# Kernel optimization log

Hardware: AMD Instinct MI355X
Metric: run time of the kernel (lower is better)

## Reference

```python
import jax, jax.numpy as jnp
import numpy as np

NUM_HEADS = 16
D_MODEL = 1024
DK = D_MODEL // NUM_HEADS


def setup_inputs() -> dict:
    key = jax.random.key(0)
    kH, kq, kk, kv, ko = jax.random.split(key, 5)
    scale = 0.02
    return {
        "H": jax.random.normal(kH, (4, 2048, D_MODEL), dtype=jnp.float32),
        "Wq": jax.random.normal(kq, (D_MODEL, D_MODEL), dtype=jnp.float32) * scale,
        "Wk": jax.random.normal(kk, (D_MODEL, D_MODEL), dtype=jnp.float32) * scale,
        "Wv": jax.random.normal(kv, (D_MODEL, D_MODEL), dtype=jnp.float32) * scale,
        "Wo": jax.random.normal(ko, (D_MODEL, D_MODEL), dtype=jnp.float32) * scale,
    }


def reference(H, Wq, Wk, Wv, Wo):
    b, T, d = H.shape
    n, dk = NUM_HEADS, DK
    # projections -> [b, n, T, dk]
    def split_heads(x):
        return x.reshape(b, T, n, dk).transpose(0, 2, 1, 3)
    Q = split_heads(H @ Wq)
    K = split_heads(H @ Wk)
    V = split_heads(H @ Wv)
    scores = jnp.einsum("bntd,bnsd->bnts", Q, K) / jnp.sqrt(jnp.float32(dk))
    causal = jnp.tril(jnp.ones((T, T), dtype=bool))
    scores = jnp.where(causal[None, None], scores, -jnp.inf)
    attn = jax.nn.softmax(scores, axis=-1)  # dropout rate 0 -> identity
    out = jnp.einsum("bnts,bnsd->bntd", attn, V)  # [b, n, T, dk]
    out = out.transpose(0, 2, 1, 3).reshape(b, T, n * dk)
    return out @ Wo
```

## Files before the change

### kernel.cpp

```cpp
#include <hip/hip_runtime.h>
#include <hip/hip_bf16.h>

#define T_SEQ 2048
#define DM 1024
#define DM2 2048
#define NH 16
#define DKH 64
#define NBATCH 4
#define MROWS (NBATCH*T_SEQ)

typedef __attribute__((ext_vector_type(8))) short bf16x8;
typedef __attribute__((ext_vector_type(4))) short bf16x4;
typedef __attribute__((ext_vector_type(4))) float f32x4;
typedef __attribute__((ext_vector_type(4))) unsigned short u16x4;

#define NEG_INF (-__builtin_inff())

#if __has_builtin(__builtin_amdgcn_exp2f)
#define EXP2(x) __builtin_amdgcn_exp2f(x)
#else
#define EXP2(x) exp2f(x)
#endif

static __device__ __forceinline__ unsigned short f2bf(float f){
  union { float f; unsigned u; } v; v.f = f;
  unsigned r = v.u + 0x7fffu + ((v.u >> 16) & 1u);
  return (unsigned short)(r >> 16);
}

static __device__ __forceinline__ unsigned short f2bfc(float f){
  union { __hip_bfloat16 h; unsigned short u; } cv;
  cv.h = __float2bfloat16(f);
  return cv.u;
}

static __device__ __forceinline__ void gload_lds16(const void* g, void* l){
  __builtin_amdgcn_global_load_lds(
      (const __attribute__((address_space(1))) void*)g,
      (__attribute__((address_space(3))) void*)l, 16, 0, 0);
}

__global__ void convh(const float4* __restrict__ in, u16x4* __restrict__ out, int n4){
  for (int i = blockIdx.x*blockDim.x + threadIdx.x; i < n4; i += gridDim.x*blockDim.x){
    float4 v = in[i];
    u16x4 o;
    o[0] = f2bf(v.x); o[1] = f2bf(v.y); o[2] = f2bf(v.z); o[3] = f2bf(v.w);
    out[i] = o;
  }
}

__global__ void convw(const float* __restrict__ W0, const float* __restrict__ W1,
                      const float* __restrict__ W2, const float* __restrict__ W3,
                      unsigned short* __restrict__ O0, unsigned short* __restrict__ O1,
                      unsigned short* __restrict__ O2, unsigned short* __restrict__ O3)
{
  const float* W = (blockIdx.z==0)?W0:(blockIdx.z==1)?W1:(blockIdx.z==2)?W2:W3;
  unsigned short* O = (blockIdx.z==0)?O0:(blockIdx.z==1)?O1:(blockIdx.z==2)?O2:O3;
  const float sc = (blockIdx.z==0) ? 0.18033688f : 1.0f;
  __shared__ float t[32][33];
  const int nx = blockIdx.x*32, kx = blockIdx.y*32;
  const int tx = threadIdx.x, ty = threadIdx.y;
  #pragma unroll
  for (int i = 0; i < 4; ++i)
    t[ty + i*8][tx] = W[(size_t)(kx + ty + i*8)*DM + nx + tx];
  __syncthreads();
  #pragma unroll
  for (int i = 0; i < 4; ++i)
    O[(size_t)(nx + ty + i*8)*DM + kx + tx] = f2bf(t[tx][ty + i*8] * sc);
}

template<bool F32OUT>
__global__ __launch_bounds__(256) void gemm_bt(const unsigned short* __restrict__ A,
                                               const unsigned short* __restrict__ Bt,
                                               void* __restrict__ Cp,
                                               int M, int N, int K)
{
  __shared__ __attribute__((aligned(16))) unsigned short a_lds[128*64];
  __shared__ __attribute__((aligned(16))) unsigned short b_lds[128*64];
  const int tid = threadIdx.x;
  const int w = tid >> 6, l = tid & 63;
  const int g = l >> 4, lr = l & 15;
  const int wr = w >> 1, wc = w & 1;
  const int m0 = blockIdx.x * 128, n0 = blockIdx.y * 128;
  f32x4 acc[4][4] = {};
  const int nk = K >> 6;
  for (int ks = 0; ks < nk; ++ks){
    __syncthreads();
    const int k0 = ks << 6;
    #pragma unroll
    for (int i = 0; i < 4; ++i){
      int c = (w*4 + i)*64 + l;
      int row = c >> 3;
      int gc = (c & 7) ^ (row & 7);
      gload_lds16(A + (size_t)(m0 + row)*K + (k0 + gc*8), &a_lds[c*8]);
    }
    #pragma unroll
    for (int i = 0; i < 4; ++i){
      int c = (w*4 + i)*64 + l;
      int row = c >> 3;
      int gc = (c & 7) ^ (row & 7);
      gload_lds16(Bt + (size_t)(n0 + row)*K + (k0 + gc*8), &b_lds[c*8]);
    }
    __syncthreads();
    #pragma unroll
    for (int kc = 0; kc < 2; ++kc){
      bf16x8 af[4], bf_[4];
      #pragma unroll
      for (int mt = 0; mt < 4; ++mt){
        int row = wr*64 + mt*16 + lr;
        int off = row*128 + ((kc*64 + g*16) ^ ((row & 7) << 4));
        af[mt] = *(const bf16x8*)((const char*)a_lds + off);
      }
      #pragma unroll
      for (int nt = 0; nt < 4; ++nt){
        int row = wc*64 + nt*16 + lr;
        int off = row*128 + ((kc*64 + g*16) ^ ((row & 7) << 4));
        bf_[nt] = *(const bf16x8*)((const char*)b_lds + off);
      }
      #pragma unroll
      for (int mt = 0; mt < 4; ++mt)
        #pragma unroll
        for (int nt = 0; nt < 4; ++nt)
          acc[mt][nt] = __builtin_amdgcn_mfma_f32_16x16x32_bf16(af[mt], bf_[nt], acc[mt][nt], 0, 0, 0);
    }
  }
  #pragma unroll
  for (int mt = 0; mt < 4; ++mt){
    #pragma unroll
    for (int nt = 0; nt < 4; ++nt){
      const int col = n0 + wc*64 + nt*16 + lr;
      #pragma unroll
      for (int r = 0; r < 4; ++r){
        const int row = m0 + wr*64 + mt*16 + 4*g + r;
        if (F32OUT) ((float*)Cp)[(size_t)row*N + col] = acc[mt][nt][r];
        else ((unsigned short*)Cp)[(size_t)row*N + col] = f2bf(acc[mt][nt][r]);
      }
    }
  }
}

static __device__ __forceinline__ void softmax_tile8(
    f32x4 (&s)[8], float& m_run, float& l_run, f32x4 (&acc)[4],
    bf16x4 (&pb)[8], int j0, int qg, int g, bool fullTile)
{
  if (!fullTile){
    #pragma unroll
    for (int kc = 0; kc < 8; ++kc)
      #pragma unroll
      for (int r = 0; r < 4; ++r){
        int kvg = j0 + kc*16 + 4*g + r;
        s[kc][r] = (kvg <= qg) ? s[kc][r] : NEG_INF;
      }
  }
  float m4[8];
  #pragma unroll
  for (int kc = 0; kc < 8; ++kc)
    m4[kc] = fmaxf(fmaxf(s[kc][0], s[kc][1]), fmaxf(s[kc][2], s[kc][3]));
  float tm = fmaxf(fmaxf(fmaxf(m4[0], m4[1]), fmaxf(m4[2], m4[3])),
                   fmaxf(fmaxf(m4[4], m4[5]), fmaxf(m4[6], m4[7])));
  tm = fmaxf(tm, __shfl_xor(tm, 16));
  tm = fmaxf(tm, __shfl_xor(tm, 32));
  float mm;
  if (__all(tm - m_run <= 8.f)){
    mm = m_run;
  } else {
    const float m_new = fmaxf(m_run, tm);
    const float fac = EXP2(m_run - m_new);
    l_run *= fac;
    m_run = m_new; mm = m_new;
    #pragma unroll
    for (int mt = 0; mt < 4; ++mt){
      acc[mt][0] *= fac; acc[mt][1] *= fac; acc[mt][2] *= fac; acc[mt][3] *= fac;
    }
  }
  float ps0 = 0.f, ps1 = 0.f, ps2 = 0.f, ps3 = 0.f;
  #pragma unroll
  for (int kc = 0; kc < 8; ++kc){
    float e0 = EXP2(s[kc][0] - mm); float e1 = EXP2(s[kc][1] - mm);
    float e2 = EXP2(s[kc][2] - mm); float e3 = EXP2(s[kc][3] - mm);
    s[kc][0] = e0; s[kc][1] = e1; s[kc][2] = e2; s[kc][3] = e3;
    ps0 += e0; ps1 += e1; ps2 += e2; ps3 += e3;
  }
  float ps = (ps0 + ps1) + (ps2 + ps3);
  ps += __shfl_xor(ps, 16);
  ps += __shfl_xor(ps, 32);
  l_run += ps;
  #pragma unroll
  for (int kc = 0; kc < 8; ++kc){
    bf16x4 t;
    t[0] = (short)f2bfc(s[kc][0]); t[1] = (short)f2bfc(s[kc][1]);
    t[2] = (short)f2bfc(s[kc][2]); t[3] = (short)f2bfc(s[kc][3]);
    pb[kc] = t;
  }
}

__global__ __launch_bounds__(512, 4) void attn_kernel(const unsigned short* __restrict__ QK,
                                                      const unsigned short* __restrict__ Vt,
                                                      unsigned short* __restrict__ Og)
{
  __shared__ __attribute__((aligned(16))) unsigned short k_lds[2][128*64];
  __shared__ __attribute__((aligned(16))) unsigned short v_lds[2][64*128];
  const int tid = threadIdx.x;
  const int w = tid >> 6, l = tid & 63;
  const int g = l >> 4, lr = l & 15;
  const int L = blockIdx.x;
  const int xcd = L & 7, idx = L >> 3;
  const int bh = xcd*8 + (idx & 7);
  const int pair = idx >> 3;
  const int b = bh >> 4, h = bh & 15;
  const size_t baseK = (size_t)(b*T_SEQ)*DM2 + 1024 + h*DKH;
  const size_t baseV = (size_t)(h*DKH)*MROWS + (size_t)b*T_SEQ;

  const int cA = tid, cB = tid + 512;
  const int krA = cA >> 3, kgA = (cA & 7) ^ (krA & 7);
  const int krB = cB >> 3, kgB = (cB & 7) ^ (krB & 7);
  const int vrA = cA >> 4, vgA = (cA & 15) ^ (vrA & 15);
  const int vrB = cB >> 4, vgB = (cB & 15) ^ (vrB & 15);

  auto STAGE = [&](int jt, int buf){
    const int j0s = jt * 128;
    gload_lds16(QK + baseK + (size_t)(j0s + krA)*DM2 + kgA*8, &k_lds[buf][cA*8]);
    gload_lds16(QK + baseK + (size_t)(j0s + krB)*DM2 + kgB*8, &k_lds[buf][cB*8]);
    gload_lds16(Vt + baseV + (size_t)vrA*MROWS + j0s + vgA*8, &v_lds[buf][cA*8]);
    gload_lds16(Vt + baseV + (size_t)vrB*MROWS + j0s + vgB*8, &v_lds[buf][cB*8]);
  };

  #pragma unroll 1
  for (int seg = 0; seg < 2; ++seg){
    const int qblk = seg ? pair : (15 - pair);
    const int q0 = qblk * 128;
    const int qlo = q0 + w*16;
    const int qg = qlo + lr;
    const size_t rowQ = (size_t)(b*T_SEQ + qg)*DM2 + h*DKH;
    bf16x8 qf[2];
    qf[0] = *(const bf16x8*)(QK + rowQ + g*8);
    qf[1] = *(const bf16x8*)(QK + rowQ + 32 + g*8);
    float m_run = NEG_INF, l_run = 0.f;
    f32x4 acc[4] = {};
    const int ntiles = qblk + 1;

    STAGE(0, 0);
    __syncthreads();

    for (int jt = 0; jt < ntiles; ++jt){
      const int cur = jt & 1;
      if (jt + 1 < ntiles) STAGE(jt + 1, cur ^ 1);
      const int j0 = jt * 128;

      f32x4 s[8];
      __builtin_amdgcn_s_setprio(1);
      #pragma unroll
      for (int kc = 0; kc < 8; ++kc){
        f32x4 z = {};
        #pragma unroll
        for (int c2 = 0; c2 < 2; ++c2){
          int row = kc*16 + lr;
          int off = row*128 + ((c2*64 + g*16) ^ ((row & 7) << 4));
          bf16x8 kf = *(const bf16x8*)((const char*)k_lds[cur] + off);
          z = __builtin_amdgcn_mfma_f32_16x16x32_bf16(kf, qf[c2], z, 0, 0, 0);
        }
        s[kc] = z;
      }
      __builtin_amdgcn_s_setprio(0);
      bf16x4 pb[8];
      softmax_tile8(s, m_run, l_run, acc, pb, j0, qg, g, jt < qblk);
      __builtin_amdgcn_s_setprio(1);
      #pragma unroll
      for (int mt = 0; mt < 4; ++mt){
        const int vrow = mt*16 + lr;
        #pragma unroll
        for (int kc = 0; kc < 8; ++kc){
          const int voff = vrow*256 + ((((kc<<1) + (g>>1)) ^ (vrow & 15)) << 4) + ((g & 1) << 3);
          bf16x4 vf = *(const bf16x4*)((const char*)v_lds[cur] + voff);
          acc[mt] = __builtin_amdgcn_mfma_f32_16x16x16bf16_1k(vf, pb[kc], acc[mt], 0, 0, 0);
        }
      }
      __builtin_amdgcn_s_setprio(0);
      __syncthreads();
    }
    const float inv = 1.f / l_run;
    const size_t rowO = (size_t)(b*T_SEQ + qg)*DM + h*DKH;
    #pragma unroll
    for (int mt = 0; mt < 4; ++mt){
      unsigned u0 = (unsigned)f2bfc(acc[mt][0]*inv) | ((unsigned)f2bfc(acc[mt][1]*inv) << 16);
      unsigned u1 = (unsigned)f2bfc(acc[mt][2]*inv) | ((unsigned)f2bfc(acc[mt][3]*inv) << 16);
      *(unsigned*)(Og + rowO + mt*16 + 4*g)     = u0;
      *(unsigned*)(Og + rowO + mt*16 + 4*g + 2) = u1;
    }
  }
}

extern "C" void kernel_launch(void* const* d_in, const int* in_sizes, int n_in,
                              void* d_out, int out_size, void* d_ws, size_t ws_size,
                              hipStream_t stream)
{
  (void)in_sizes; (void)n_in; (void)out_size; (void)ws_size;
  const float* H  = (const float*)d_in[0];
  const float* Wq = (const float*)d_in[1];
  const float* Wk = (const float*)d_in[2];
  const float* Wv = (const float*)d_in[3];
  const float* Wo = (const float*)d_in[4];
  char* ws = (char*)d_ws;
  unsigned short* Hb   = (unsigned short*)(ws);
  unsigned short* Wqkt = (unsigned short*)(ws + 16777216);
  unsigned short* Wkt  = (unsigned short*)(ws + 18874368);
  unsigned short* Wvt  = (unsigned short*)(ws + 20971520);
  unsigned short* Wot  = (unsigned short*)(ws + 23068672);
  unsigned short* QKb  = (unsigned short*)(ws + 25165824);
  unsigned short* Vtb  = (unsigned short*)(ws + 58720256);
  unsigned short* Ab   = (unsigned short*)(ws + 75497472);

  convh<<<2048, 256, 0, stream>>>((const float4*)H, (u16x4*)Hb, MROWS*DM/4);
  convw<<<dim3(32,32,4), dim3(32,8), 0, stream>>>(Wq, Wk, Wv, Wo, Wqkt, Wkt, Wvt, Wot);
  gemm_bt<false><<<dim3(64,16), 256, 0, stream>>>(Hb, Wqkt, QKb, MROWS, DM2, DM);
  gemm_bt<false><<<dim3(8,64), 256, 0, stream>>>(Wvt, Hb, Vtb, DM, MROWS, DM);
  attn_kernel<<<dim3(512), 512, 0, stream>>>(QKb, Vtb, Ab);
  gemm_bt<true><<<dim3(64,8), 256, 0, stream>>>(Ab, Wot, d_out, MROWS, DM, DM);
}
```

Before: 181.7 us.

## Merge prep and QKV GEMM launches, compute softmax denominator via MFMA, unroll attention loop

Merges the H and weight conversion kernels into one launch, and merges the QK and V-transpose GEMMs into a single grid, removing two launches and their tail gaps. In attention, the running row sum is no longer built with VALU adds and cross-lane shuffles. A fifth accumulator instead receives an extra MFMA against a ones vector, so the denominator comes out of the matrix unit. The KV loop is also unrolled by two with compile-time buffer indices. The ones-MFMA sums bf16-rounded probabilities rather than fp32 ones, which slightly changes numerics.

```diff
diff --git a/kernel.cpp b/kernel.cpp
--- a/kernel.cpp
+++ b/kernel.cpp
@@ -40,48 +40,51 @@
       (__attribute__((address_space(3))) void*)l, 16, 0, 0);
 }
 
-__global__ void convh(const float4* __restrict__ in, u16x4* __restrict__ out, int n4){
-  for (int i = blockIdx.x*blockDim.x + threadIdx.x; i < n4; i += gridDim.x*blockDim.x){
-    float4 v = in[i];
-    u16x4 o;
-    o[0] = f2bf(v.x); o[1] = f2bf(v.y); o[2] = f2bf(v.z); o[3] = f2bf(v.w);
-    out[i] = o;
-  }
-}
-
-__global__ void convw(const float* __restrict__ W0, const float* __restrict__ W1,
-                      const float* __restrict__ W2, const float* __restrict__ W3,
-                      unsigned short* __restrict__ O0, unsigned short* __restrict__ O1,
-                      unsigned short* __restrict__ O2, unsigned short* __restrict__ O3)
-{
-  const float* W = (blockIdx.z==0)?W0:(blockIdx.z==1)?W1:(blockIdx.z==2)?W2:W3;
-  unsigned short* O = (blockIdx.z==0)?O0:(blockIdx.z==1)?O1:(blockIdx.z==2)?O2:O3;
-  const float sc = (blockIdx.z==0) ? 0.18033688f : 1.0f;
+__global__ __launch_bounds__(256) void convprep(
+    const float* __restrict__ H,
+    const float* __restrict__ W0, const float* __restrict__ W1,
+    const float* __restrict__ W2, const float* __restrict__ W3,
+    u16x4* __restrict__ Hb4,
+    unsigned short* __restrict__ O0, unsigned short* __restrict__ O1,
+    unsigned short* __restrict__ O2, unsigned short* __restrict__ O3)
+{
   __shared__ float t[32][33];
-  const int nx = blockIdx.x*32, kx = blockIdx.y*32;
-  const int tx = threadIdx.x, ty = threadIdx.y;
-  #pragma unroll
-  for (int i = 0; i < 4; ++i)
-    t[ty + i*8][tx] = W[(size_t)(kx + ty + i*8)*DM + nx + tx];
-  __syncthreads();
-  #pragma unroll
-  for (int i = 0; i < 4; ++i)
-    O[(size_t)(nx + ty + i*8)*DM + kx + tx] = f2bf(t[tx][ty + i*8] * sc);
+  const int bid = blockIdx.x, tid = threadIdx.x;
+  if (bid < 4096){
+    const int z = bid >> 10, rem = bid & 1023;
+    const int nx = (rem & 31)*32, kx = (rem >> 5)*32;
+    const float* W = (z==0)?W0:(z==1)?W1:(z==2)?W2:W3;
+    unsigned short* O = (z==0)?O0:(z==1)?O1:(z==2)?O2:O3;
+    const float sc = (z==0) ? 0.18033688f : 1.0f;
+    const int tx = tid & 31, ty = tid >> 5;
+    #pragma unroll
+    for (int i = 0; i < 4; ++i)
+      t[ty + i*8][tx] = W[(size_t)(kx + ty + i*8)*DM + nx + tx];
+    __syncthreads();
+    #pragma unroll
+    for (int i = 0; i < 4; ++i)
+      O[(size_t)(nx + ty + i*8)*DM + kx + tx] = f2bf(t[tx][ty + i*8] * sc);
+  } else {
+    const int n4 = MROWS*DM/4;
+    for (int i = (bid - 4096)*256 + tid; i < n4; i += 2048*256){
+      float4 v = ((const float4*)H)[i];
+      u16x4 o;
+      o[0] = f2bf(v.x); o[1] = f2bf(v.y); o[2] = f2bf(v.z); o[3] = f2bf(v.w);
+      Hb4[i] = o;
+    }
+  }
 }
 
 template<bool F32OUT>
-__global__ __launch_bounds__(256) void gemm_bt(const unsigned short* __restrict__ A,
-                                               const unsigned short* __restrict__ Bt,
-                                               void* __restrict__ Cp,
-                                               int M, int N, int K)
-{
-  __shared__ __attribute__((aligned(16))) unsigned short a_lds[128*64];
-  __shared__ __attribute__((aligned(16))) unsigned short b_lds[128*64];
+static __device__ __forceinline__ void gemm_body(
+    const unsigned short* __restrict__ A, const unsigned short* __restrict__ Bt,
+    void* __restrict__ Cp, int N, int K, int m0, int n0,
+    unsigned short* a_lds, unsigned short* b_lds)
+{
   const int tid = threadIdx.x;
   const int w = tid >> 6, l = tid & 63;
   const int g = l >> 4, lr = l & 15;
   const int wr = w >> 1, wc = w & 1;
-  const int m0 = blockIdx.x * 128, n0 = blockIdx.y * 128;
   f32x4 acc[4][4] = {};
   const int nk = K >> 6;
   for (int ks = 0; ks < nk; ++ks){
@@ -139,8 +142,37 @@
   }
 }
 
+__global__ __launch_bounds__(256) void gemm_qkv(
+    const unsigned short* __restrict__ Hb, const unsigned short* __restrict__ Wqkt,
+    unsigned short* __restrict__ QKb,
+    const unsigned short* __restrict__ Wvt, unsigned short* __restrict__ Vtb)
+{
+  __shared__ __attribute__((aligned(16))) unsigned short a_lds[128*64];
+  __shared__ __attribute__((aligned(16))) unsigned short b_lds[128*64];
+  const int bid = blockIdx.x;
+  const unsigned short *A, *Bt; unsigned short* Cp; int N, m0, n0;
+  if (bid < 1024){
+    A = Hb; Bt = Wqkt; Cp = QKb; N = DM2;
+    m0 = (bid & 63)*128; n0 = (bid >> 6)*128;
+  } else {
+    const int t2 = bid - 1024;
+    A = Wvt; Bt = Hb; Cp = Vtb; N = MROWS;
+    m0 = (t2 & 7)*128; n0 = (t2 >> 3)*128;
+  }
+  gemm_body<false>(A, Bt, Cp, N, DM, m0, n0, a_lds, b_lds);
+}
+
+__global__ __launch_bounds__(256) void gemm_out(
+    const unsigned short* __restrict__ Ab, const unsigned short* __restrict__ Wot,
+    float* __restrict__ Out)
+{
+  __shared__ __attribute__((aligned(16))) unsigned short a_lds[128*64];
+  __shared__ __attribute__((aligned(16))) unsigned short b_lds[128*64];
+  gemm_body<true>(Ab, Wot, Out, DM, DM, blockIdx.x*128, blockIdx.y*128, a_lds, b_lds);
+}
+
 static __device__ __forceinline__ void softmax_tile8(
-    f32x4 (&s)[8], float& m_run, float& l_run, f32x4 (&acc)[4],
+    f32x4 (&s)[8], float& m_run, f32x4 (&acc)[5],
     bf16x4 (&pb)[8], int j0, int qg, int g, bool fullTile)
 {
   if (!fullTile){
@@ -166,30 +198,19 @@
   } else {
     const float m_new = fmaxf(m_run, tm);
     const float fac = EXP2(m_run - m_new);
-    l_run *= fac;
     m_run = m_new; mm = m_new;
     #pragma unroll
-    for (int mt = 0; mt < 4; ++mt){
+    for (int mt = 0; mt < 5; ++mt){
       acc[mt][0] *= fac; acc[mt][1] *= fac; acc[mt][2] *= fac; acc[mt][3] *= fac;
     }
   }
-  float ps0 = 0.f, ps1 = 0.f, ps2 = 0.f, ps3 = 0.f;
   #pragma unroll
   for (int kc = 0; kc < 8; ++kc){
     float e0 = EXP2(s[kc][0] - mm); float e1 = EXP2(s[kc][1] - mm);
     float e2 = EXP2(s[kc][2] - mm); float e3 = EXP2(s[kc][3] - mm);
-    s[kc][0] = e0; s[kc][1] = e1; s[kc][2] = e2; s[kc][3] = e3;
-    ps0 += e0; ps1 += e1; ps2 += e2; ps3 += e3;
-  }
-  float ps = (ps0 + ps1) + (ps2 + ps3);
-  ps += __shfl_xor(ps, 16);
-  ps += __shfl_xor(ps, 32);
-  l_run += ps;
-  #pragma unroll
-  for (int kc = 0; kc < 8; ++kc){
     bf16x4 t;
-    t[0] = (short)f2bfc(s[kc][0]); t[1] = (short)f2bfc(s[kc][1]);
-    t[2] = (short)f2bfc(s[kc][2]); t[3] = (short)f2bfc(s[kc][3]);
+    t[0] = (short)f2bfc(e0); t[1] = (short)f2bfc(e1);
+    t[2] = (short)f2bfc(e2); t[3] = (short)f2bfc(e3);
     pb[kc] = t;
   }
 }
@@ -210,6 +231,7 @@
   const int b = bh >> 4, h = bh & 15;
   const size_t baseK = (size_t)(b*T_SEQ)*DM2 + 1024 + h*DKH;
   const size_t baseV = (size_t)(h*DKH)*MROWS + (size_t)b*T_SEQ;
+  const bf16x4 vone = {(short)0x3F80, (short)0x3F80, (short)0x3F80, (short)0x3F80};
 
   const int cA = tid, cB = tid + 512;
   const int krA = cA >> 3, kgA = (cA & 7) ^ (krA & 7);
@@ -225,60 +247,71 @@
     gload_lds16(Vt + baseV + (size_t)vrB*MROWS + j0s + vgB*8, &v_lds[buf][cB*8]);
   };
 
+#define ROUND(JT, CUR) do{                                                       \
+    const int jt_ = (JT);                                                        \
+    if (jt_ + 1 < ntiles) STAGE(jt_ + 1, (CUR)^1);                               \
+    const int j0_ = jt_ * 128;                                                   \
+    f32x4 s[8];                                                                  \
+    __builtin_amdgcn_s_setprio(1);                                               \
+    _Pragma("unroll")                                                            \
+    for (int kc = 0; kc < 8; ++kc){                                              \
+      f32x4 z = {};                                                              \
+      _Pragma("unroll")                                                          \
+      for (int c2 = 0; c2 < 2; ++c2){                                            \
+        int row = kc*16 + lr;                                                    \
+        int off = row*128 + ((c2*64 + g*16) ^ ((row & 7) << 4));                 \
+        bf16x8 kf = *(const bf16x8*)((const char*)k_lds[CUR] + off);             \
+        z = __builtin_amdgcn_mfma_f32_16x16x32_bf16(kf, qf[c2], z, 0, 0, 0);     \
+      }                                                                          \
+      s[kc] = z;                                                                 \
+    }                                                                            \
+    __builtin_amdgcn_s_setprio(0);                                               \
+    bf16x4 pb[8];                                                                \
+    softmax_tile8(s, m_run, acc, pb, j0_, qg, g, jt_ < qblk);                    \
+    __builtin_amdgcn_s_setprio(1);                                               \
+    _Pragma("unroll")                                                            \
+    for (int mt = 0; mt < 4; ++mt){                                              \
+      const int vrow = mt*16 + lr;                                               \
+      _Pragma("unroll")                                                          \
+      for (int kc = 0; kc < 8; ++kc){                                            \
+        const int voff = vrow*256 + ((((kc<<1) + (g>>1)) ^ (vrow & 15)) << 4)    \
+                         + ((g & 1) << 3);                                       \
+        bf16x4 vf = *(const bf16x4*)((const char*)v_lds[CUR] + voff);            \
+        acc[mt] = __builtin_amdgcn_mfma_f32_16x16x16bf16_1k(vf, pb[kc], acc[mt], 0, 0, 0); \
+      }                                                                          \
+    }                                                                            \
+    _Pragma("unroll")                                                            \
+    for (int kc = 0; kc < 8; ++kc)                                               \
+      acc[4] = __builtin_amdgcn_mfma_f32_16x16x16bf16_1k(vone, pb[kc], acc[4], 0, 0, 0); \
+    __builtin_amdgcn_s_setprio(0);                                               \
+    __syncthreads();                                                             \
+  } while(0)
+
   #pragma unroll 1
   for (int seg = 0; seg < 2; ++seg){
     const int qblk = seg ? pair : (15 - pair);
     const int q0 = qblk * 128;
-    const int qlo = q0 + w*16;
-    const int qg = qlo + lr;
+    const int qg = q0 + w*16 + lr;
     const size_t rowQ = (size_t)(b*T_SEQ + qg)*DM2 + h*DKH;
     bf16x8 qf[2];
     qf[0] = *(const bf16x8*)(QK + rowQ + g*8);
     qf[1] = *(const bf16x8*)(QK + rowQ + 32 + g*8);
-    float m_run = NEG_INF, l_run = 0.f;
-    f32x4 acc[4] = {};
+    float m_run = NEG_INF;
+    f32x4 acc[5] = {};
     const int ntiles = qblk + 1;
 
     STAGE(0, 0);
     __syncthreads();
 
-    for (int jt = 0; jt < ntiles; ++jt){
-      const int cur = jt & 1;
-      if (jt + 1 < ntiles) STAGE(jt + 1, cur ^ 1);
-      const int j0 = jt * 128;
-
-      f32x4 s[8];
-      __builtin_amdgcn_s_setprio(1);
-      #pragma unroll
-      for (int kc = 0; kc < 8; ++kc){
-        f32x4 z = {};
-        #pragma unroll
-        for (int c2 = 0; c2 < 2; ++c2){
-          int row = kc*16 + lr;
-          int off = row*128 + ((c2*64 + g*16) ^ ((row & 7) << 4));
-          bf16x8 kf = *(const bf16x8*)((const char*)k_lds[cur] + off);
-          z = __builtin_amdgcn_mfma_f32_16x16x32_bf16(kf, qf[c2], z, 0, 0, 0);
-        }
-        s[kc] = z;
-      }
-      __builtin_amdgcn_s_setprio(0);
-      bf16x4 pb[8];
-      softmax_tile8(s, m_run, l_run, acc, pb, j0, qg, g, jt < qblk);
-      __builtin_amdgcn_s_setprio(1);
-      #pragma unroll
-      for (int mt = 0; mt < 4; ++mt){
-        const int vrow = mt*16 + lr;
-        #pragma unroll
-        for (int kc = 0; kc < 8; ++kc){
-          const int voff = vrow*256 + ((((kc<<1) + (g>>1)) ^ (vrow & 15)) << 4) + ((g & 1) << 3);
-          bf16x4 vf = *(const bf16x4*)((const char*)v_lds[cur] + voff);
-          acc[mt] = __builtin_amdgcn_mfma_f32_16x16x16bf16_1k(vf, pb[kc], acc[mt], 0, 0, 0);
-        }
-      }
-      __builtin_amdgcn_s_setprio(0);
-      __syncthreads();
-    }
-    const float inv = 1.f / l_run;
+    int jt = 0;
+    #pragma unroll 1
+    for (; jt + 2 <= ntiles; jt += 2){
+      ROUND(jt, 0);
+      ROUND(jt + 1, 1);
+    }
+    if (jt < ntiles) ROUND(jt, 0);
+
+    const float inv = 1.f / acc[4][0];
     const size_t rowO = (size_t)(b*T_SEQ + qg)*DM + h*DKH;
     #pragma unroll
     for (int mt = 0; mt < 4; ++mt){
@@ -288,6 +321,7 @@
       *(unsigned*)(Og + rowO + mt*16 + 4*g + 2) = u1;
     }
   }
+#undef ROUND
 }
 
 extern "C" void kernel_launch(void* const* d_in, const int* in_sizes, int n_in,
@@ -310,10 +344,9 @@
   unsigned short* Vtb  = (unsigned short*)(ws + 58720256);
   unsigned short* Ab   = (unsigned short*)(ws + 75497472);
 
-  convh<<<2048, 256, 0, stream>>>((const float4*)H, (u16x4*)Hb, MROWS*DM/4);
-  convw<<<dim3(32,32,4), dim3(32,8), 0, stream>>>(Wq, Wk, Wv, Wo, Wqkt, Wkt, Wvt, Wot);
-  gemm_bt<false><<<dim3(64,16), 256, 0, stream>>>(Hb, Wqkt, QKb, MROWS, DM2, DM);
-  gemm_bt<false><<<dim3(8,64), 256, 0, stream>>>(Wvt, Hb, Vtb, DM, MROWS, DM);
+  convprep<<<6144, 256, 0, stream>>>(H, Wq, Wk, Wv, Wo,
+                                     (u16x4*)Hb, Wqkt, Wkt, Wvt, Wot);
+  gemm_qkv<<<1536, 256, 0, stream>>>(Hb, Wqkt, QKb, Wvt, Vtb);
   attn_kernel<<<dim3(512), 512, 0, stream>>>(QKb, Vtb, Ab);
-  gemm_bt<true><<<dim3(64,8), 256, 0, stream>>>(Ab, Wot, d_out, MROWS, DM, DM);
-}
+  gemm_out<<<dim3(64,8), 256, 0, stream>>>(Ab, Wot, (float*)d_out);
+}
```

New measurement: 171.2 us. 5.8% less time.
